# Performance work log

Hardware: AMD Instinct MI355X
Metric: run time of the kernel (lower is better)

The kernel has to match this reference:

```python
import jax, jax.numpy as jnp
import numpy as np

QTZ_BETA = 0.25


def setup_inputs() -> dict:
    key = jax.random.key(0)
    k1, k2 = jax.random.split(key)
    z = jax.random.normal(k1, (65536, 1, 256), dtype=jnp.float32)
    codebook = jax.random.normal(k2, (4096, 256), dtype=jnp.float32)
    return {"z": z, "codebook": codebook}


def reference(z, codebook):
    """Hard VQ quantization: nearest-codebook lookup with straight-through
    estimator plus codebook commitment loss. Returns (z_q, codebook_loss,
    min_embed_ids)."""
    D = codebook.shape[-1]
    z_f = z.reshape(-1, D)  # [N, D]
    # Pairwise squared L2 distances via expansion: ||z||^2 - 2 z c^T + ||c||^2
    # (argmin is invariant to the monotone transform vs. torch.cdist's sqrt)
    d2 = (
        jnp.sum(z_f * z_f, axis=1, keepdims=True)  # [N, 1]
        - 2.0 * (z_f @ codebook.T)                 # [N, K]
        + jnp.sum(codebook * codebook, axis=1)     # [K]
    )
    min_embed_ids = jnp.argmin(d2, axis=1)  # [N]
    # one_hot @ codebook is exactly a gather of codebook rows
    z_q = jnp.take(codebook, min_embed_ids, axis=0).reshape(z.shape)
    # Straight-through estimator
    z_q = z + jax.lax.stop_gradient(z_q - z)
    # Codebook loss (uses the STE z_q, matching the torch code)
    codebook_loss = (
        jnp.mean((jax.lax.stop_gradient(z_q) - z) ** 2)
        + jnp.mean((z_q - jax.lax.stop_gradient(z)) ** 2) * QTZ_BETA
    )
    return (z_q, codebook_loss, min_embed_ids)
```

## Files before the change

kernel.cpp:

```cpp
#include <hip/hip_runtime.h>
#include <stdint.h>

typedef _Float16 f16;
typedef _Float16 f16x4 __attribute__((ext_vector_type(4)));
typedef _Float16 f16x8 __attribute__((ext_vector_type(8)));
typedef float f32x4 __attribute__((ext_vector_type(4)));
typedef unsigned long long u64;

#define D_DIM 256
#define K_CB 4096
#define N_ROWS 65536
#define BM 128
#define BN 128
#define N_TILES 32
#define LOSS_OFF 16777216
#define IDS_OFF 16777217
#define MAX_FIX 4096

#define WS_CHI 0
#define WS_CN 2097152
#define WS_CNT 2113536
#define WS_ROWS 2113600
#define WS_SLOTS 2129984

#define GL_LDS(g, s_) __builtin_amdgcn_global_load_lds( \
    (const __attribute__((address_space(1))) void*)(g), \
    (__attribute__((address_space(3))) void*)(s_), 16, 0, 0)

static __device__ __forceinline__ uint32_t f2u(float x) { union { float f; uint32_t u; } c; c.f = x; return c.u; }
static __device__ __forceinline__ float u2f(uint32_t x) { union { float f; uint32_t u; } c; c.u = x; return c.f; }
static __device__ __forceinline__ uint32_t umin_(uint32_t a, uint32_t b) { return a < b ? a : b; }
static __device__ __forceinline__ uint32_t umax_(uint32_t a, uint32_t b) { return a > b ? a : b; }
static __device__ __forceinline__ u64 d2u(double x) { union { double d; u64 u; } c; c.d = x; return c.u; }

__global__ __launch_bounds__(256) void k_prep_cb(const float* __restrict__ cb,
                                                 f16* __restrict__ chi,
                                                 float* __restrict__ cn,
                                                 uint32_t* __restrict__ cnt,
                                                 u64* __restrict__ slots,
                                                 float* __restrict__ loss_slot) {
    const int tid = threadIdx.x;
    const int w = tid >> 6, l = tid & 63;
    const int row = blockIdx.x * 4 + w;
    const float4 v = ((const float4*)cb)[row * 64 + l];
    f16x4 h4;
    h4[0] = (f16)v.x; h4[1] = (f16)v.y; h4[2] = (f16)v.z; h4[3] = (f16)v.w;
    float ss = v.x * v.x + v.y * v.y + v.z * v.z + v.w * v.w;
#pragma unroll
    for (int m = 32; m >= 1; m >>= 1) ss += __shfl_xor(ss, m);
    ((f16x4*)chi)[row * 64 + l] = h4;
    if (l == 0) cn[row] = ss;
    if (tid < 4) slots[blockIdx.x * 4 + tid] = 0xFFFFFFFFFFFFFFFFull;
    if (blockIdx.x == 0 && tid == 0) { *cnt = 0; *loss_slot = 0.0f; }
}

__global__ __launch_bounds__(256) void k_main(const float* __restrict__ z,
                                              const float* __restrict__ cb,
                                              const f16* __restrict__ chi,
                                              const float* __restrict__ cn,
                                              uint32_t* __restrict__ cnt,
                                              uint32_t* __restrict__ rows,
                                              float* __restrict__ out) {
    extern __shared__ char smem[];
    const int tid = threadIdx.x;
    const int w = tid >> 6, l = tid & 63;
    const int wm = w >> 1, wn = w & 1;
    const int l15 = l & 15, qh = l >> 4;
    const int blk = blockIdx.x;
    const float* ztile = z + (size_t)blk * (BM * D_DIM);

#pragma unroll 4
    for (int p = 0; p < 32; ++p) {
        const int r = p * 4 + w;
        const float4 v = ((const float4*)ztile)[r * 64 + l];
        f16x4 h4;
        h4[0] = (f16)(v.x * -2.0f); h4[1] = (f16)(v.y * -2.0f);
        h4[2] = (f16)(v.z * -2.0f); h4[3] = (f16)(v.w * -2.0f);
        const int addr = r * 512 + ((((l >> 1) ^ (r & 7))) << 4) + ((l & 1) << 3);
        *(f16x4*)(smem + addr) = h4;
    }

    float cnNext[4];
#pragma unroll
    for (int j = 0; j < 4; ++j) cnNext[j] = cn[wn * 64 + j * 16 + l15];

    const int e0 = tid >> 2;
    const int q0 = (tid & 3) ^ ((e0 >> 1) & 3);
    const int offE = e0 * 256 + q0 * 8;

    int rowb[4], rs[4], bcon[4];
#pragma unroll
    for (int i = 0; i < 4; ++i) {
        const int r = wm * 64 + i * 16 + l15;
        rowb[i] = r * 512;
        rs[i] = r & 7;
    }
#pragma unroll
    for (int j = 0; j < 4; ++j) {
        const int e = wn * 64 + j * 16 + l15;
        bcon[j] = e * 64 + ((qh ^ ((e >> 1) & 3)) << 4);
    }

    {
        const f16* gh = chi + offE;
        char* bb = smem + 65536 + w * 1024;
        GL_LDS(gh, bb);
        GL_LDS(gh + 16384, bb + 4096);
    }

    uint32_t k1[16], k2[16], k3[16];
#pragma unroll
    for (int s = 0; s < 16; ++s) { k1[s] = 0xFFFFFFFFu; k2[s] = 0xFFFFFFFFu; k3[s] = 0xFFFFFFFFu; }
    f32x4 acc[4][4];
    float cnCur[4];

    for (int tile = 0; tile < N_TILES; ++tile) {
#pragma unroll
        for (int j = 0; j < 4; ++j) cnCur[j] = cnNext[j];
#pragma unroll
        for (int j = 0; j < 4; ++j) {
            const float base = cnCur[j] + 64.0f;
#pragma unroll
            for (int i = 0; i < 4; ++i) acc[i][j] = (f32x4){base, base, base, base};
        }
#pragma unroll
        for (int kc = 0; kc < 8; ++kc) {
            __syncthreads();
            const int step = tile * 8 + kc;
            if (step + 1 < N_TILES * 8) {
                const int nt = (step + 1) >> 3, nk = (step + 1) & 7;
                const f16* gh = chi + nt * (BN * D_DIM) + nk * 32 + offE;
                char* bb = smem + 65536 + ((step + 1) & 1) * 8192 + w * 1024;
                GL_LDS(gh, bb);
                GL_LDS(gh + 16384, bb + 4096);
            }
            if (kc == 0) {
                const int tn = (tile + 1 < N_TILES) ? tile + 1 : tile;
#pragma unroll
                for (int j = 0; j < 4; ++j)
                    cnNext[j] = cn[tn * BN + wn * 64 + j * 16 + l15];
            }
            const char* bbase = smem + 65536 + (step & 1) * 8192;
            f16x8 ah[4], bh[4];
#pragma unroll
            for (int i = 0; i < 4; ++i) {
                const int t = ((kc << 2) + qh) ^ rs[i];
                ah[i] = *(const f16x8*)(smem + rowb[i] + (t << 4));
            }
#pragma unroll
            for (int j = 0; j < 4; ++j) bh[j] = *(const f16x8*)(bbase + bcon[j]);
#pragma unroll
            for (int i = 0; i < 4; ++i)
#pragma unroll
                for (int j = 0; j < 4; ++j)
                    acc[i][j] = __builtin_amdgcn_mfma_f32_16x16x32_f16(ah[i], bh[j], acc[i][j], 0, 0, 0);
        }
        const int colb = tile * BN + wn * 64 + l15;
#pragma unroll
        for (int j = 0; j < 4; ++j) {
            const uint32_t col = (uint32_t)(colb + j * 16);
#pragma unroll
            for (int i = 0; i < 4; ++i)
#pragma unroll
                for (int rr = 0; rr < 4; ++rr) {
                    const int s = i * 4 + rr;
                    const uint32_t kk = (f2u(acc[i][j][rr]) & 0xFFFFF000u) | col;
                    const uint32_t t2 = umax_(k1[s], kk); k1[s] = umin_(k1[s], kk);
                    const uint32_t t3 = umax_(k2[s], t2); k2[s] = umin_(k2[s], t2);
                    k3[s] = umin_(k3[s], t3);
                }
        }
    }

#pragma unroll
    for (int s = 0; s < 16; ++s) {
        uint32_t a1 = k1[s], a2 = k2[s], a3 = k3[s];
#pragma unroll
        for (int m = 1; m <= 8; m <<= 1) {
            const uint32_t b1 = (uint32_t)__shfl_xor((int)a1, m);
            const uint32_t b2 = (uint32_t)__shfl_xor((int)a2, m);
            const uint32_t b3 = (uint32_t)__shfl_xor((int)a3, m);
            const uint32_t x = umax_(a1, b1);
            const uint32_t m2v = umin_(a2, b2), M2 = umax_(a2, b2);
            const uint32_t m3v = umin_(a3, b3);
            a1 = umin_(a1, b1);
            a2 = umin_(x, m2v);
            a3 = umin_(umin_(umax_(x, m2v), M2), m3v);
        }
        k1[s] = a1; k2[s] = a2; k3[s] = a3;
    }
    __syncthreads();
    uint32_t* mk = (uint32_t*)(smem + 65536);
    double* lossW = (double*)(smem + 65536 + 1536);
    if (wn == 0 && l15 == 0) {
#pragma unroll
        for (int s = 0; s < 16; ++s) {
            const int row = wm * 64 + (s >> 2) * 16 + qh * 4 + (s & 3);
            mk[row] = k1[s]; mk[128 + row] = k2[s]; mk[256 + row] = k3[s];
        }
    }
    __syncthreads();
    if (wn == 1 && l15 == 0) {
#pragma unroll
        for (int s = 0; s < 16; ++s) {
            const int row = wm * 64 + (s >> 2) * 16 + qh * 4 + (s & 3);
            const uint32_t b1 = mk[row], b2 = mk[128 + row], b3 = mk[256 + row];
            const uint32_t x = umax_(k1[s], b1);
            const uint32_t m2v = umin_(k2[s], b2), M2 = umax_(k2[s], b2);
            const uint32_t m3v = umin_(k3[s], b3);
            mk[row] = umin_(k1[s], b1);
            mk[128 + row] = umin_(x, m2v);
            mk[256 + row] = umin_(umin_(umax_(x, m2v), M2), m3v);
        }
    }
    __syncthreads();

    double lossAcc = 0.0;
    for (int it = 0; it < 32; ++it) {
        const int row = it * 4 + w;
        const uint32_t K1 = mk[row], K2 = mk[128 + row], K3 = mk[256 + row];
        const int col1 = (int)(K1 & 4095u), col2 = (int)(K2 & 4095u);
        const float4 c1 = ((const float4*)cb)[col1 * 64 + l];
        const float4 c2 = ((const float4*)cb)[col2 * 64 + l];
        const float4 z4 = ((const float4*)ztile)[row * 64 + l];
        double e1, e2;
        {
            const double dx1 = (double)c1.x - z4.x, dy1 = (double)c1.y - z4.y;
            const double dz1 = (double)c1.z - z4.z, dw1 = (double)c1.w - z4.w;
            e1 = dx1 * dx1 + dy1 * dy1 + dz1 * dz1 + dw1 * dw1;
            const double dx2 = (double)c2.x - z4.x, dy2 = (double)c2.y - z4.y;
            const double dz2 = (double)c2.z - z4.z, dw2 = (double)c2.w - z4.w;
            e2 = dx2 * dx2 + dy2 * dy2 + dz2 * dz2 + dw2 * dw2;
        }
        float zn2 = z4.x * z4.x + z4.y * z4.y + z4.z * z4.z + z4.w * z4.w;
#pragma unroll
        for (int m = 32; m >= 1; m >>= 1) {
            e1 += __shfl_xor(e1, m);
            e2 += __shfl_xor(e2, m);
            zn2 += __shfl_xor(zn2, m);
        }
        const bool take1 = (e1 < e2) || (e1 == e2 && col1 <= col2);
        const float4 cw = take1 ? c1 : c2;
        ((float4*)out)[(blk * BM + row) * 64 + l] = cw;
        if (l == 0) {
            const int colw = take1 ? col1 : col2;
            const double ew = take1 ? e1 : e2;
            out[IDS_OFF + blk * BM + row] = (float)colw;
            lossAcc += ew;
            const float d3 = u2f(K3 & 0xFFFFF000u) + zn2 - 64.0f;
            const float eps = 0.006f * sqrtf(zn2) + 0.01f;
            if (!((float)ew < d3 - eps)) {
                const uint32_t e = atomicAdd(cnt, 1u);
                if (e < MAX_FIX) rows[e] = (uint32_t)(blk * BM + row);
            }
        }
    }
    if (l == 0) lossW[w] = lossAcc;
    __syncthreads();
    if (tid == 0) {
        const double tot = (lossW[0] + lossW[1] + lossW[2] + lossW[3]) * (1.25 / 16777216.0);
        atomicAdd(out + LOSS_OFF, (float)tot);
    }
}

__global__ __launch_bounds__(256) void k_fix_scan(const float* __restrict__ z,
                                                  const float* __restrict__ cb,
                                                  const uint32_t* __restrict__ cnt,
                                                  const uint32_t* __restrict__ rows,
                                                  u64* __restrict__ slots) {
    __shared__ float zrow[256];
    __shared__ u64 wmin[4];
    const int tid = threadIdx.x;
    const int w = tid >> 6, l = tid & 63;
    const int chunk = blockIdx.x & 15;
    uint32_t n = *cnt; if (n > MAX_FIX) n = MAX_FIX;
    for (uint32_t e = blockIdx.x >> 4; e < n; e += 64) {
        const int row = (int)rows[e];
        __syncthreads();
        if (tid < 64) ((float4*)zrow)[tid] = ((const float4*)z)[row * 64 + tid];
        __syncthreads();
        const int c = chunk * 256 + tid;
        const float4* crow = (const float4*)(cb + (size_t)c * 256);
        double s = 0.0;
        for (int q = 0; q < 64; ++q) {
            const float4 cv = crow[q];
            const float4 zv = ((const float4*)zrow)[q];
            const double dx = (double)cv.x - zv.x, dy = (double)cv.y - zv.y;
            const double dz = (double)cv.z - zv.z, dw = (double)cv.w - zv.w;
            s += dx * dx + dy * dy + dz * dz + dw * dw;
        }
        u64 key = (d2u(s) & 0xFFFFFFFFFFFFF000ull) | (u64)c;
#pragma unroll
        for (int m = 32; m >= 1; m >>= 1) {
            const u64 o = __shfl_xor(key, m);
            if (o < key) key = o;
        }
        if (l == 0) wmin[w] = key;
        __syncthreads();
        if (tid == 0) {
            u64 k = wmin[0];
            if (wmin[1] < k) k = wmin[1];
            if (wmin[2] < k) k = wmin[2];
            if (wmin[3] < k) k = wmin[3];
            atomicMin(&slots[e], k);
        }
    }
}

__global__ __launch_bounds__(256) void k_fix_patch(const float* __restrict__ z,
                                                   const float* __restrict__ cb,
                                                   const uint32_t* __restrict__ cnt,
                                                   const uint32_t* __restrict__ rows,
                                                   const u64* __restrict__ slots,
                                                   float* __restrict__ out) {
    const int tid = threadIdx.x;
    uint32_t n = *cnt; if (n > MAX_FIX) n = MAX_FIX;
    for (uint32_t e = blockIdx.x; e < n; e += 256) {
        const int row = (int)rows[e];
        const int newc = (int)(slots[e] & 4095ull);
        const int oldc = (int)out[IDS_OFF + row];
        if (newc == oldc) continue;
        double dOld = 0.0, dNew = 0.0;
        if (tid < 64) {
            const float4 zv = ((const float4*)z)[row * 64 + tid];
            const float4 co = ((const float4*)cb)[oldc * 64 + tid];
            const float4 cn4 = ((const float4*)cb)[newc * 64 + tid];
            const double ax = (double)co.x - zv.x, ay = (double)co.y - zv.y;
            const double az = (double)co.z - zv.z, aw = (double)co.w - zv.w;
            dOld = ax * ax + ay * ay + az * az + aw * aw;
            const double bx = (double)cn4.x - zv.x, by = (double)cn4.y - zv.y;
            const double bz = (double)cn4.z - zv.z, bw = (double)cn4.w - zv.w;
            dNew = bx * bx + by * by + bz * bz + bw * bw;
            ((float4*)out)[row * 64 + tid] = cn4;
        }
#pragma unroll
        for (int m = 32; m >= 1; m >>= 1) {
            dOld += __shfl_xor(dOld, m);
            dNew += __shfl_xor(dNew, m);
        }
        if (tid == 0) {
            out[IDS_OFF + row] = (float)newc;
            atomicAdd(out + LOSS_OFF, (float)((dNew - dOld) * (1.25 / 16777216.0)));
        }
    }
}

extern "C" void kernel_launch(void* const* d_in, const int* in_sizes, int n_in,
                              void* d_out, int out_size, void* d_ws, size_t ws_size,
                              hipStream_t stream) {
    (void)in_sizes; (void)n_in; (void)out_size; (void)ws_size;
    const float* z = (const float*)d_in[0];
    const float* cb = (const float*)d_in[1];
    float* out = (float*)d_out;
    char* ws = (char*)d_ws;
    f16* chi = (f16*)(ws + WS_CHI);
    float* cn = (float*)(ws + WS_CN);
    uint32_t* cnt = (uint32_t*)(ws + WS_CNT);
    uint32_t* rows = (uint32_t*)(ws + WS_ROWS);
    u64* slots = (u64*)(ws + WS_SLOTS);

    hipFuncSetAttribute((const void*)k_main,
                        hipFuncAttributeMaxDynamicSharedMemorySize, 81920);

    k_prep_cb<<<K_CB / 4, 256, 0, stream>>>(cb, chi, cn, cnt, slots, out + LOSS_OFF);
    k_main<<<N_ROWS / BM, 256, 81920, stream>>>(z, cb, chi, cn, cnt, rows, out);
    k_fix_scan<<<1024, 256, 0, stream>>>(z, cb, cnt, rows, slots);
    k_fix_patch<<<256, 256, 0, stream>>>(z, cb, cnt, rows, slots, out);
}
```

Measured before the change: 304.2 us.

## Shrink row tile to 64 with per-wave 16x128 strips and med3 top-3 tracking

The row block per workgroup drops from 128 to 64. Each of the four waves now owns 16 rows across all 128 codebook columns instead of a 64x64 quadrant, which removes the cross-wave top-3 merge and halves LDS use. Top-3 insertion now uses v_med3_u32 in place of a min/max chain. Twice as many workgroups run, which may help occupancy and tail balance. In exchange, each codebook tile staged in LDS is reused by fewer rows, so LDS traffic per MFMA rises (8 B-loads per A-load) and codebook global reads double.

```diff
diff --git a/kernel.cpp b/kernel.cpp
--- a/kernel.cpp
+++ b/kernel.cpp
@@ -10,7 +10,7 @@
 #define D_DIM 256
 #define K_CB 4096
 #define N_ROWS 65536
-#define BM 128
+#define BM 64
 #define BN 128
 #define N_TILES 32
 #define LOSS_OFF 16777216
@@ -23,6 +23,7 @@
 #define WS_ROWS 2113600
 #define WS_SLOTS 2129984
 
+
 #define GL_LDS(g, s_) __builtin_amdgcn_global_load_lds( \
     (const __attribute__((address_space(1))) void*)(g), \
     (__attribute__((address_space(3))) void*)(s_), 16, 0, 0)
@@ -32,6 +33,11 @@
 static __device__ __forceinline__ uint32_t umin_(uint32_t a, uint32_t b) { return a < b ? a : b; }
 static __device__ __forceinline__ uint32_t umax_(uint32_t a, uint32_t b) { return a > b ? a : b; }
 static __device__ __forceinline__ u64 d2u(double x) { union { double d; u64 u; } c; c.d = x; return c.u; }
+static __device__ __forceinline__ uint32_t med3u(uint32_t a, uint32_t b, uint32_t c) {
+    uint32_t d;
+    asm("v_med3_u32 %0, %1, %2, %3" : "=v"(d) : "v"(a), "v"(b), "v"(c));
+    return d;
+}
 
 __global__ __launch_bounds__(256) void k_prep_cb(const float* __restrict__ cb,
                                                  f16* __restrict__ chi,
@@ -64,13 +70,12 @@
     extern __shared__ char smem[];
     const int tid = threadIdx.x;
     const int w = tid >> 6, l = tid & 63;
-    const int wm = w >> 1, wn = w & 1;
     const int l15 = l & 15, qh = l >> 4;
     const int blk = blockIdx.x;
     const float* ztile = z + (size_t)blk * (BM * D_DIM);
 
 #pragma unroll 4
-    for (int p = 0; p < 32; ++p) {
+    for (int p = 0; p < 16; ++p) {
         const int r = p * 4 + w;
         const float4 v = ((const float4*)ztile)[r * 64 + l];
         f16x4 h4;
@@ -80,48 +85,40 @@
         *(f16x4*)(smem + addr) = h4;
     }
 
-    float cnNext[4];
-#pragma unroll
-    for (int j = 0; j < 4; ++j) cnNext[j] = cn[wn * 64 + j * 16 + l15];
+    float cnNext[8];
+#pragma unroll
+    for (int j = 0; j < 8; ++j) cnNext[j] = cn[j * 16 + l15];
 
     const int e0 = tid >> 2;
     const int q0 = (tid & 3) ^ ((e0 >> 1) & 3);
     const int offE = e0 * 256 + q0 * 8;
 
-    int rowb[4], rs[4], bcon[4];
-#pragma unroll
-    for (int i = 0; i < 4; ++i) {
-        const int r = wm * 64 + i * 16 + l15;
-        rowb[i] = r * 512;
-        rs[i] = r & 7;
-    }
-#pragma unroll
-    for (int j = 0; j < 4; ++j) {
-        const int e = wn * 64 + j * 16 + l15;
+    const int rA = w * 16 + l15;
+    const int rowb = rA * 512, rs = rA & 7;
+    int bcon[8];
+#pragma unroll
+    for (int j = 0; j < 8; ++j) {
+        const int e = j * 16 + l15;
         bcon[j] = e * 64 + ((qh ^ ((e >> 1) & 3)) << 4);
     }
 
     {
         const f16* gh = chi + offE;
-        char* bb = smem + 65536 + w * 1024;
+        char* bb = smem + 32768 + w * 1024;
         GL_LDS(gh, bb);
         GL_LDS(gh + 16384, bb + 4096);
     }
 
-    uint32_t k1[16], k2[16], k3[16];
-#pragma unroll
-    for (int s = 0; s < 16; ++s) { k1[s] = 0xFFFFFFFFu; k2[s] = 0xFFFFFFFFu; k3[s] = 0xFFFFFFFFu; }
-    f32x4 acc[4][4];
-    float cnCur[4];
+    uint32_t k1[4], k2[4], k3[4];
+#pragma unroll
+    for (int s = 0; s < 4; ++s) { k1[s] = 0xFFFFFFFFu; k2[s] = 0xFFFFFFFFu; k3[s] = 0xFFFFFFFFu; }
+    f32x4 acc[8];
 
     for (int tile = 0; tile < N_TILES; ++tile) {
 #pragma unroll
-        for (int j = 0; j < 4; ++j) cnCur[j] = cnNext[j];
-#pragma unroll
-        for (int j = 0; j < 4; ++j) {
-            const float base = cnCur[j] + 64.0f;
-#pragma unroll
-            for (int i = 0; i < 4; ++i) acc[i][j] = (f32x4){base, base, base, base};
+        for (int j = 0; j < 8; ++j) {
+            const float base = cnNext[j] + 64.0f;
+            acc[j] = (f32x4){base, base, base, base};
         }
 #pragma unroll
         for (int kc = 0; kc < 8; ++kc) {
@@ -130,50 +127,42 @@
             if (step + 1 < N_TILES * 8) {
                 const int nt = (step + 1) >> 3, nk = (step + 1) & 7;
                 const f16* gh = chi + nt * (BN * D_DIM) + nk * 32 + offE;
-                char* bb = smem + 65536 + ((step + 1) & 1) * 8192 + w * 1024;
+                char* bb = smem + 32768 + ((step + 1) & 1) * 8192 + w * 1024;
                 GL_LDS(gh, bb);
                 GL_LDS(gh + 16384, bb + 4096);
             }
             if (kc == 0) {
                 const int tn = (tile + 1 < N_TILES) ? tile + 1 : tile;
 #pragma unroll
-                for (int j = 0; j < 4; ++j)
-                    cnNext[j] = cn[tn * BN + wn * 64 + j * 16 + l15];
+                for (int j = 0; j < 8; ++j)
+                    cnNext[j] = cn[tn * BN + j * 16 + l15];
             }
-            const char* bbase = smem + 65536 + (step & 1) * 8192;
-            f16x8 ah[4], bh[4];
-#pragma unroll
-            for (int i = 0; i < 4; ++i) {
-                const int t = ((kc << 2) + qh) ^ rs[i];
-                ah[i] = *(const f16x8*)(smem + rowb[i] + (t << 4));
+            const char* bbase = smem + 32768 + (step & 1) * 8192;
+            const int t = ((kc << 2) + qh) ^ rs;
+            const f16x8 ah = *(const f16x8*)(smem + rowb + (t << 4));
+            f16x8 bh[8];
+#pragma unroll
+            for (int j = 0; j < 8; ++j) bh[j] = *(const f16x8*)(bbase + bcon[j]);
+#pragma unroll
+            for (int j = 0; j < 8; ++j)
+                acc[j] = __builtin_amdgcn_mfma_f32_16x16x32_f16(ah, bh[j], acc[j], 0, 0, 0);
+        }
+        const uint32_t colb = (uint32_t)(tile * BN + l15);
+#pragma unroll
+        for (int j = 0; j < 8; ++j) {
+            const uint32_t col = colb + j * 16;
+#pragma unroll
+            for (int rr = 0; rr < 4; ++rr) {
+                const uint32_t kk = (f2u(acc[j][rr]) & 0xFFFFF000u) | col;
+                k3[rr] = med3u(k2[rr], k3[rr], kk);
+                k2[rr] = med3u(k1[rr], k2[rr], kk);
+                k1[rr] = umin_(k1[rr], kk);
             }
-#pragma unroll
-            for (int j = 0; j < 4; ++j) bh[j] = *(const f16x8*)(bbase + bcon[j]);
-#pragma unroll
-            for (int i = 0; i < 4; ++i)
-#pragma unroll
-                for (int j = 0; j < 4; ++j)
-                    acc[i][j] = __builtin_amdgcn_mfma_f32_16x16x32_f16(ah[i], bh[j], acc[i][j], 0, 0, 0);
-        }
-        const int colb = tile * BN + wn * 64 + l15;
-#pragma unroll
-        for (int j = 0; j < 4; ++j) {
-            const uint32_t col = (uint32_t)(colb + j * 16);
-#pragma unroll
-            for (int i = 0; i < 4; ++i)
-#pragma unroll
-                for (int rr = 0; rr < 4; ++rr) {
-                    const int s = i * 4 + rr;
-                    const uint32_t kk = (f2u(acc[i][j][rr]) & 0xFFFFF000u) | col;
-                    const uint32_t t2 = umax_(k1[s], kk); k1[s] = umin_(k1[s], kk);
-                    const uint32_t t3 = umax_(k2[s], t2); k2[s] = umin_(k2[s], t2);
-                    k3[s] = umin_(k3[s], t3);
-                }
-        }
-    }
-
-#pragma unroll
-    for (int s = 0; s < 16; ++s) {
+        }
+    }
+
+#pragma unroll
+    for (int s = 0; s < 4; ++s) {
         uint32_t a1 = k1[s], a2 = k2[s], a3 = k3[s];
 #pragma unroll
         for (int m = 1; m <= 8; m <<= 1) {
@@ -190,35 +179,21 @@
         k1[s] = a1; k2[s] = a2; k3[s] = a3;
     }
     __syncthreads();
-    uint32_t* mk = (uint32_t*)(smem + 65536);
-    double* lossW = (double*)(smem + 65536 + 1536);
-    if (wn == 0 && l15 == 0) {
-#pragma unroll
-        for (int s = 0; s < 16; ++s) {
-            const int row = wm * 64 + (s >> 2) * 16 + qh * 4 + (s & 3);
-            mk[row] = k1[s]; mk[128 + row] = k2[s]; mk[256 + row] = k3[s];
+    uint32_t* mk = (uint32_t*)(smem + 32768);
+    double* lossW = (double*)(smem + 32768 + 768);
+    if (l15 == 0) {
+#pragma unroll
+        for (int rr = 0; rr < 4; ++rr) {
+            const int row = w * 16 + qh * 4 + rr;
+            mk[row] = k1[rr]; mk[64 + row] = k2[rr]; mk[128 + row] = k3[rr];
         }
     }
     __syncthreads();
-    if (wn == 1 && l15 == 0) {
-#pragma unroll
-        for (int s = 0; s < 16; ++s) {
-            const int row = wm * 64 + (s >> 2) * 16 + qh * 4 + (s & 3);
-            const uint32_t b1 = mk[row], b2 = mk[128 + row], b3 = mk[256 + row];
-            const uint32_t x = umax_(k1[s], b1);
-            const uint32_t m2v = umin_(k2[s], b2), M2 = umax_(k2[s], b2);
-            const uint32_t m3v = umin_(k3[s], b3);
-            mk[row] = umin_(k1[s], b1);
-            mk[128 + row] = umin_(x, m2v);
-            mk[256 + row] = umin_(umin_(umax_(x, m2v), M2), m3v);
-        }
-    }
-    __syncthreads();
 
     double lossAcc = 0.0;
-    for (int it = 0; it < 32; ++it) {
+    for (int it = 0; it < 16; ++it) {
         const int row = it * 4 + w;
-        const uint32_t K1 = mk[row], K2 = mk[128 + row], K3 = mk[256 + row];
+        const uint32_t K1 = mk[row], K2 = mk[64 + row], K3 = mk[128 + row];
         const int col1 = (int)(K1 & 4095u), col2 = (int)(K2 & 4095u);
         const float4 c1 = ((const float4*)cb)[col1 * 64 + l];
         const float4 c2 = ((const float4*)cb)[col2 * 64 + l];
@@ -359,11 +334,8 @@
     uint32_t* rows = (uint32_t*)(ws + WS_ROWS);
     u64* slots = (u64*)(ws + WS_SLOTS);
 
-    hipFuncSetAttribute((const void*)k_main,
-                        hipFuncAttributeMaxDynamicSharedMemorySize, 81920);
-
     k_prep_cb<<<K_CB / 4, 256, 0, stream>>>(cb, chi, cn, cnt, slots, out + LOSS_OFF);
-    k_main<<<N_ROWS / BM, 256, 81920, stream>>>(z, cb, chi, cn, cnt, rows, out);
+    k_main<<<N_ROWS / BM, 256, 49152, stream>>>(z, cb, chi, cn, cnt, rows, out);
     k_fix_scan<<<1024, 256, 0, stream>>>(z, cb, cnt, rows, slots);
     k_fix_patch<<<256, 256, 0, stream>>>(z, cb, cnt, rows, slots, out);
 }
```

Measured after the change: 359.5 us. 1.18x slower.
